# Performance work log

Hardware: AMD Instinct MI355X
Metric: run time of the kernel (lower is better)

The kernel has to match this reference:

```python
import jax, jax.numpy as jnp
import numpy as np

N_NODES = 30000
DEGREE = 16
HIDDEN = 128
MSG = 128


def setup_inputs() -> dict:
    key = jax.random.key(0)
    ks = jax.random.split(key, 16)
    coords = jax.random.normal(ks[0], (N_NODES, 3), dtype=jnp.float32)
    hidden = jax.random.normal(ks[1], (N_NODES, HIDDEN), dtype=jnp.float32)
    # fixed in-degree ring graph: unique (src,dst) pairs, in-degree == DEGREE for all nodes
    dst = jnp.repeat(jnp.arange(N_NODES, dtype=jnp.int64), DEGREE)
    off = jnp.tile(jnp.arange(1, DEGREE + 1, dtype=jnp.int64), N_NODES)
    src = (dst + off) % N_NODES
    edges = jnp.stack([src, dst], axis=0)  # [2, E]
    s = 0.05
    W1 = jax.random.normal(ks[2], (2 * HIDDEN + 1, MSG), dtype=jnp.float32) * s
    b1 = jnp.zeros((MSG,), jnp.float32)
    W2 = jax.random.normal(ks[3], (MSG, MSG), dtype=jnp.float32) * s
    b2 = jnp.zeros((MSG,), jnp.float32)
    Wa = jax.random.normal(ks[4], (MSG, 1), dtype=jnp.float32) * s
    ba = jnp.zeros((1,), jnp.float32)
    Wc1 = jax.random.normal(ks[5], (MSG, MSG), dtype=jnp.float32) * s
    bc1 = jnp.zeros((MSG,), jnp.float32)
    Wc2 = jax.random.normal(ks[6], (MSG, 1), dtype=jnp.float32) * s  # original zero-inits; random for nontrivial baseline
    Wh1 = jax.random.normal(ks[7], (HIDDEN + MSG, MSG), dtype=jnp.float32) * s
    bh1 = jnp.zeros((MSG,), jnp.float32)
    Wh2 = jax.random.normal(ks[8], (MSG, HIDDEN), dtype=jnp.float32) * s
    bh2 = jnp.zeros((HIDDEN,), jnp.float32)
    return dict(coords=coords, hidden=hidden, edges=edges, W1=W1, b1=b1, W2=W2, b2=b2,
                Wa=Wa, ba=ba, Wc1=Wc1, bc1=bc1, Wc2=Wc2, Wh1=Wh1, bh1=bh1, Wh2=Wh2, bh2=bh2)


def reference(coords, hidden, edges, W1, b1, W2, b2, Wa, ba, Wc1, bc1, Wc2, Wh1, bh1, Wh2, bh2):
    n = coords.shape[0]
    src, dst = edges[0], edges[1]
    coords_dif = coords[src] - coords[dst]                      # [E,3]
    l2 = jnp.linalg.norm(coords_dif, axis=1, keepdims=True)     # [E,1]
    x = jnp.concatenate([hidden[src], hidden[dst], l2], axis=1)  # [E, 2h+1]
    m = jnp.tanh(x @ W1 + b1)
    m = jnp.tanh(m @ W2 + b2)                                   # m_ij [E,MSG]
    m = jax.nn.sigmoid(m @ Wa + ba) * m                          # attention gate
    c = jnp.tanh(m @ Wc1 + bc1)
    c = jnp.tanh(c @ Wc2)                                       # [E,1] (Tanh since has_attention)
    coord_trans = coords_dif * c                                 # [E,3]
    # dense [N,N,*] scatter + sum over dim 0 == segment-sum over edges[1] (unique edges)
    trans_sum = jax.ops.segment_sum(coord_trans, dst, num_segments=n)  # [N,3]
    indeg = jax.ops.segment_sum(jnp.ones_like(dst, dtype=coords.dtype), dst, num_segments=n)
    coords_out = coords + trans_sum / indeg[:, None]
    m_i = jax.ops.segment_sum(m, dst, num_segments=n)            # [N,MSG]
    h = jnp.tanh(jnp.concatenate([hidden, m_i], axis=1) @ Wh1 + bh1)
    h = h @ Wh2 + bh2
    hidden_out = hidden + h
    return coords_out, hidden_out
```

## Files before the change

### kernel.cpp

```cpp
#include <hip/hip_runtime.h>
#include <hip/hip_bf16.h>
#include <math.h>


typedef __attribute__((ext_vector_type(8))) short short8;
typedef __attribute__((ext_vector_type(4))) float f32x4;
typedef __attribute__((ext_vector_type(4))) unsigned int u32x4;

#define MFMA __builtin_amdgcn_mfma_f32_16x16x32_bf16

#define OFF_W1A_HI 0
#define OFF_W1A_LO 16384
#define OFF_W1B_HI 32768
#define OFF_W1B_LO 49152
#define OFF_W2_HI  65536
#define OFF_WC1_HI 81920
#define OFF_WH1_HI 98304
#define OFF_WH1_LO 131072
#define OFF_WH2_HI 163840
#define FRAG_TOTAL 180224

__device__ __align__(16) unsigned short g_frags[FRAG_TOTAL];

#define DEVFN static __device__ __forceinline__

DEVFN unsigned short f2bf(float x) {
  unsigned int u = __float_as_uint(x);
  u += 0x7fffu + ((u >> 16) & 1u);
  return (unsigned short)(u >> 16);
}
DEVFN float bf2f(unsigned short h) { return __uint_as_float(((unsigned int)h) << 16); }

DEVFN unsigned int pk2(float a, float b) {
  __hip_bfloat162 p = __float22bfloat162_rn(make_float2(a, b));
  union { __hip_bfloat162 h; unsigned int u; } cv;
  cv.h = p;
  return cv.u;
}

DEVFN float ftanh(float x) {
  float e = exp2f(x * 2.8853900817779268f);
  return 1.0f - 2.0f * __builtin_amdgcn_rcpf(e + 1.0f);
}
DEVFN float fsigmoid(float x) {
  float e = exp2f(-x * 1.4426950408889634f);
  return __builtin_amdgcn_rcpf(1.0f + e);
}

DEVFN short8 bfrag(int off_u16, int kt, int nt, int lane) {
  return *(const short8*)(g_frags + off_u16 + (((kt << 3) + nt) << 9) + (lane << 3));
}

DEVFN short8 xs_read(const unsigned short* Xs, int row, int sbyte) {
  return *(const short8*)((const char*)Xs + row * 256 + (sbyte ^ ((row & 7) << 4)));
}
DEVFN void xs_write8(unsigned short* Xs, int row, int cl, const float* v) {
  u32x4 w;
  w[0] = pk2(v[0], v[1]); w[1] = pk2(v[2], v[3]);
  w[2] = pk2(v[4], v[5]); w[3] = pk2(v[6], v[7]);
  *(u32x4*)((char*)Xs + row * 256 + ((cl << 4) ^ ((row & 7) << 4))) = w;
}

#define ZERO_ACC1                                                      \
  _Pragma("unroll") for (int nt = 0; nt < 8; ++nt) acc[nt] = vzero;

__global__ __launch_bounds__(256) void hconv_kernel(const float* __restrict__ h,
                                                    unsigned short* __restrict__ Hh,
                                                    unsigned short* __restrict__ Hl,
                                                    int n4) {
  int i = blockIdx.x * 256 + threadIdx.x;
  if (i >= n4) return;
  f32x4 v = ((const f32x4*)h)[i];
  unsigned short hh[4], ll[4];
#pragma unroll
  for (int j = 0; j < 4; ++j) {
    hh[j] = f2bf(v[j]);
    ll[j] = f2bf(v[j] - bf2f(hh[j]));
  }
  ((uint2*)Hh)[i] = make_uint2(hh[0] | ((unsigned)hh[1] << 16), hh[2] | ((unsigned)hh[3] << 16));
  ((uint2*)Hl)[i] = make_uint2(ll[0] | ((unsigned)ll[1] << 16), ll[2] | ((unsigned)ll[3] << 16));
}

__global__ __launch_bounds__(256) void wconv_kernel(const float* __restrict__ W1,
                                                    const float* __restrict__ W2,
                                                    const float* __restrict__ Wc1,
                                                    const float* __restrict__ Wh1,
                                                    const float* __restrict__ Wh2) {
  int t = blockIdx.x * 256 + threadIdx.x;
  if (t >= 28 * 4096) return;
  int seg = t >> 12, r = t & 4095;
  int j = r & 7, lane = (r >> 3) & 63, nt = (r >> 9) & 7;
  int kg = lane >> 4, cl = lane & 15;
  const float* src; int kt, offH, offL, perm;
  if (seg < 4)       { src = W1;             kt = seg;      offH = OFF_W1A_HI; offL = OFF_W1A_LO; perm = 0; }
  else if (seg < 8)  { src = W1 + 128 * 128; kt = seg - 4;  offH = OFF_W1B_HI; offL = OFF_W1B_LO; perm = 0; }
  else if (seg < 12) { src = W2;             kt = seg - 8;  offH = OFF_W2_HI;  offL = -1;         perm = 1; }
  else if (seg < 16) { src = Wc1;            kt = seg - 12; offH = OFF_WC1_HI; offL = -1;         perm = 1; }
  else if (seg < 24) { src = Wh1;            kt = seg - 16; offH = OFF_WH1_HI; offL = OFF_WH1_LO; perm = 0; }
  else               { src = Wh2;            kt = seg - 24; offH = OFF_WH2_HI; offL = -1;         perm = 1; }
  int ke = kt * 32 + kg * 8 + j;
  int k = perm ? ((ke & 7) * 16 + (ke >> 3)) : ke;
  float w = src[k * 128 + nt * 16 + cl];
  unsigned short h = f2bf(w);
  int fi = kt * 4096 + nt * 512 + lane * 8 + j;
  g_frags[offH + fi] = h;
  if (offL >= 0) g_frags[offL + fi] = f2bf(w - bf2f(h));
}

__global__ __launch_bounds__(256) void tdst_kernel(const unsigned short* __restrict__ Hh,
                                                   const unsigned short* __restrict__ Hl,
                                                   const float* __restrict__ b1,
                                                   float* __restrict__ T, int N) {
  const int tid = threadIdx.x, wid = tid >> 6, lane = tid & 63;
  const int cl = lane & 15, kg = lane >> 4;
  const int n0 = blockIdx.x * 64 + wid * 16;
  const int row = min(n0 + cl, N - 1) << 7;
  const f32x4 vzero = {0.f, 0.f, 0.f, 0.f};
  f32x4 acc[8];
  ZERO_ACC1;
#pragma unroll
  for (int ks = 0; ks < 4; ++ks) {
    short8 ah = *(const short8*)(Hh + row + ks * 32 + kg * 8);
    short8 al = *(const short8*)(Hl + row + ks * 32 + kg * 8);
#pragma unroll
    for (int nt = 0; nt < 8; ++nt) {
      short8 bh = bfrag(OFF_W1B_HI, ks, nt, lane);
      short8 bl = bfrag(OFF_W1B_LO, ks, nt, lane);
      acc[nt] = MFMA(ah, bh, acc[nt], 0, 0, 0);
      acc[nt] = MFMA(al, bh, acc[nt], 0, 0, 0);
      acc[nt] = MFMA(ah, bl, acc[nt], 0, 0, 0);
    }
  }
#pragma unroll
  for (int nt = 0; nt < 8; ++nt) {
    float bv = b1[nt * 16 + cl];
#pragma unroll
    for (int reg = 0; reg < 4; ++reg) {
      int rw = n0 + kg * 4 + reg;
      if (rw < N) T[(size_t)rw * 128 + nt * 16 + cl] = acc[nt][reg] + bv;
    }
  }
}

__global__ __launch_bounds__(256) void edge_kernel(
    const float* __restrict__ coords, const int* __restrict__ edges,
    const float* __restrict__ W1, const float* __restrict__ b2,
    const float* __restrict__ Wa, const float* __restrict__ ba,
    const float* __restrict__ bc1, const float* __restrict__ Wc2,
    const float* __restrict__ T, const unsigned short* __restrict__ Hh,
    const unsigned short* __restrict__ Hl, unsigned short* __restrict__ Mh,
    unsigned short* __restrict__ Ml, float* __restrict__ coords_out, int E) {
  __shared__ __align__(16) unsigned short Xs[64 * 128];
  __shared__ float sb2f[128], sbc1f[128];
  __shared__ unsigned short swl2h[128], swah[128], swc2h[128];

  const int tid = threadIdx.x, wid = tid >> 6, lane = tid & 63;
  const int cl = lane & 15, kg = lane >> 4;
  const int xrow0 = wid * 16;
  const int e0 = blockIdx.x * 64 + wid * 16;

  if (tid < 128) {
    swl2h[tid] = f2bf(W1[256 * 128 + tid]);
    swah[tid] = f2bf(Wa[tid]);
    swc2h[tid] = f2bf(Wc2[tid]);
    sb2f[tid] = b2[tid];
    sbc1f[tid] = bc1[tid];
  }
  __syncthreads();

  const int dst = edges[E + e0];
  const int src = edges[e0 + cl];
  const int srcRow = src << 7;
  const float cx = coords[3 * dst], cy = coords[3 * dst + 1], cz = coords[3 * dst + 2];
  const float dx = coords[3 * src] - cx, dy = coords[3 * src + 1] - cy, dz = coords[3 * src + 2] - cz;
  const float l2 = sqrtf(dx * dx + dy * dy + dz * dz);
  const float ba_s = ba[0];

  const f32x4 vzero = {0.f, 0.f, 0.f, 0.f};
  f32x4 acc[8];
  ZERO_ACC1;

#pragma unroll
  for (int ks = 0; ks < 4; ++ks) {
    short8 ah = *(const short8*)(Hh + srcRow + ks * 32 + kg * 8);
    short8 al = *(const short8*)(Hl + srcRow + ks * 32 + kg * 8);
#pragma unroll
    for (int nt = 0; nt < 8; ++nt) {
      short8 bh = bfrag(OFF_W1A_HI, ks, nt, lane);
      short8 bl = bfrag(OFF_W1A_LO, ks, nt, lane);
      acc[nt] = MFMA(ah, bh, acc[nt], 0, 0, 0);
      acc[nt] = MFMA(al, bh, acc[nt], 0, 0, 0);
      acc[nt] = MFMA(ah, bl, acc[nt], 0, 0, 0);
    }
  }

  {
    const float* Trow = T + (size_t)dst * 128;
    float l2r[4];
#pragma unroll
    for (int reg = 0; reg < 4; ++reg) l2r[reg] = __shfl(l2, kg * 4 + reg);
    float vv[4][8];
#pragma unroll
    for (int nt = 0; nt < 8; ++nt) {
      float tv = Trow[nt * 16 + cl];
      float wl = bf2f(swl2h[nt * 16 + cl]);
#pragma unroll
      for (int reg = 0; reg < 4; ++reg)
        vv[reg][nt] = ftanh(acc[nt][reg] + tv + l2r[reg] * wl);
    }
#pragma unroll
    for (int reg = 0; reg < 4; ++reg) xs_write8(Xs, xrow0 + kg * 4 + reg, cl, vv[reg]);
  }

  ZERO_ACC1;
#pragma unroll
  for (int ks = 0; ks < 4; ++ks) {
    short8 a = xs_read(Xs, xrow0 + cl, ks * 64 + kg * 16);
#pragma unroll
    for (int nt = 0; nt < 8; ++nt) {
      short8 b = bfrag(OFF_W2_HI, ks, nt, lane);
      acc[nt] = MFMA(a, b, acc[nt], 0, 0, 0);
    }
  }

  {
    float wac[8], b2c[8];
#pragma unroll
    for (int nt = 0; nt < 8; ++nt) {
      wac[nt] = bf2f(swah[nt * 16 + cl]);
      b2c[nt] = sb2f[nt * 16 + cl];
    }
#pragma unroll
    for (int nt = 0; nt < 8; ++nt)
#pragma unroll
      for (int reg = 0; reg < 4; ++reg)
        acc[nt][reg] = ftanh(acc[nt][reg] + b2c[nt]);
    float p[4];
#pragma unroll
    for (int reg = 0; reg < 4; ++reg) {
      float s = 0.f;
#pragma unroll
      for (int nt = 0; nt < 8; ++nt) s = fmaf(acc[nt][reg], wac[nt], s);
      p[reg] = s;
    }
#pragma unroll
    for (int m = 1; m <= 8; m <<= 1)
#pragma unroll
      for (int reg = 0; reg < 4; ++reg) p[reg] += __shfl_xor(p[reg], m);
    float g[4];
#pragma unroll
    for (int reg = 0; reg < 4; ++reg) g[reg] = fsigmoid(p[reg] + ba_s);
#pragma unroll
    for (int nt = 0; nt < 8; ++nt)
#pragma unroll
      for (int reg = 0; reg < 4; ++reg) acc[nt][reg] *= g[reg];
    float cs[8];
#pragma unroll
    for (int nt = 0; nt < 8; ++nt) {
      cs[nt] = (acc[nt][0] + acc[nt][1]) + (acc[nt][2] + acc[nt][3]);
      cs[nt] += __shfl_xor(cs[nt], 16);
      cs[nt] += __shfl_xor(cs[nt], 32);
    }
    if (lane < 16) {
      size_t base = (size_t)dst * 128 + lane;
#pragma unroll
      for (int nt = 0; nt < 8; ++nt) {
        float s = cs[nt];
        unsigned short hh = f2bf(s);
        Mh[base + nt * 16] = hh;
        Ml[base + nt * 16] = f2bf(s - bf2f(hh));
      }
    }
    float vv[4][8];
#pragma unroll
    for (int nt = 0; nt < 8; ++nt)
#pragma unroll
      for (int reg = 0; reg < 4; ++reg) vv[reg][nt] = acc[nt][reg];
#pragma unroll
    for (int reg = 0; reg < 4; ++reg) xs_write8(Xs, xrow0 + kg * 4 + reg, cl, vv[reg]);
  }

  ZERO_ACC1;
#pragma unroll
  for (int ks = 0; ks < 4; ++ks) {
    short8 a = xs_read(Xs, xrow0 + cl, ks * 64 + kg * 16);
#pragma unroll
    for (int nt = 0; nt < 8; ++nt) {
      short8 b = bfrag(OFF_WC1_HI, ks, nt, lane);
      acc[nt] = MFMA(a, b, acc[nt], 0, 0, 0);
    }
  }

  {
    float wcc[8], bcc[8];
#pragma unroll
    for (int nt = 0; nt < 8; ++nt) {
      wcc[nt] = bf2f(swc2h[nt * 16 + cl]);
      bcc[nt] = sbc1f[nt * 16 + cl];
    }
    float p[4];
#pragma unroll
    for (int reg = 0; reg < 4; ++reg) {
      float s = 0.f;
#pragma unroll
      for (int nt = 0; nt < 8; ++nt)
        s = fmaf(ftanh(acc[nt][reg] + bcc[nt]), wcc[nt], s);
      p[reg] = s;
    }
#pragma unroll
    for (int m = 1; m <= 8; m <<= 1)
#pragma unroll
      for (int reg = 0; reg < 4; ++reg) p[reg] += __shfl_xor(p[reg], m);
    float st = 0.f;
#pragma unroll
    for (int reg = 0; reg < 4; ++reg) {
      int sl = kg * 4 + reg;
      float vx = __shfl(dx, sl), vy = __shfl(dy, sl), vz = __shfl(dz, sl);
      float cmp = ((cl & 3) == 1) ? vy : (((cl & 3) == 2) ? vz : vx);
      st = fmaf(cmp, ftanh(p[reg]), st);
    }
    st += __shfl_xor(st, 16);
    st += __shfl_xor(st, 32);
    if (lane < 3)
      coords_out[dst * 3 + lane] = coords[dst * 3 + lane] + st * 0.0625f;
  }
}

__global__ __launch_bounds__(256) void node_kernel(
    const float* __restrict__ hidden, const unsigned short* __restrict__ Hh,
    const unsigned short* __restrict__ Hl, const unsigned short* __restrict__ Mh,
    const unsigned short* __restrict__ Ml, const float* __restrict__ bh1,
    const float* __restrict__ bh2, float* __restrict__ hidden_out, int N) {
  __shared__ __align__(16) unsigned short Xs[64 * 128];
  const int tid = threadIdx.x, wid = tid >> 6, lane = tid & 63;
  const int cl = lane & 15, kg = lane >> 4;
  const int xrow0 = wid * 16;
  const int n0 = blockIdx.x * 64 + wid * 16;
  const int row = min(n0 + cl, N - 1) << 7;
  const f32x4 vzero = {0.f, 0.f, 0.f, 0.f};
  f32x4 acc[8];
  ZERO_ACC1;
#pragma unroll
  for (int half = 0; half < 2; ++half) {
    const unsigned short* Ph = half ? Mh : Hh;
    const unsigned short* Pl = half ? Ml : Hl;
#pragma unroll
    for (int ks = 0; ks < 4; ++ks) {
      short8 ah = *(const short8*)(Ph + row + ks * 32 + kg * 8);
      short8 al = *(const short8*)(Pl + row + ks * 32 + kg * 8);
#pragma unroll
      for (int nt = 0; nt < 8; ++nt) {
        short8 bh = bfrag(OFF_WH1_HI, half * 4 + ks, nt, lane);
        short8 bl = bfrag(OFF_WH1_LO, half * 4 + ks, nt, lane);
        acc[nt] = MFMA(ah, bh, acc[nt], 0, 0, 0);
        acc[nt] = MFMA(al, bh, acc[nt], 0, 0, 0);
        acc[nt] = MFMA(ah, bl, acc[nt], 0, 0, 0);
      }
    }
  }
  {
    float vv[4][8];
#pragma unroll
    for (int nt = 0; nt < 8; ++nt) {
      float bv = bh1[nt * 16 + cl];
#pragma unroll
      for (int reg = 0; reg < 4; ++reg) vv[reg][nt] = ftanh(acc[nt][reg] + bv);
    }
#pragma unroll
    for (int reg = 0; reg < 4; ++reg) xs_write8(Xs, xrow0 + kg * 4 + reg, cl, vv[reg]);
  }
  ZERO_ACC1;
#pragma unroll
  for (int ks = 0; ks < 4; ++ks) {
    short8 a = xs_read(Xs, xrow0 + cl, ks * 64 + kg * 16);
#pragma unroll
    for (int nt = 0; nt < 8; ++nt) {
      short8 b = bfrag(OFF_WH2_HI, ks, nt, lane);
      acc[nt] = MFMA(a, b, acc[nt], 0, 0, 0);
    }
  }
#pragma unroll
  for (int nt = 0; nt < 8; ++nt) {
    float bv = bh2[nt * 16 + cl];
#pragma unroll
    for (int reg = 0; reg < 4; ++reg) {
      int rw = n0 + kg * 4 + reg;
      if (rw < N) {
        size_t o = (size_t)rw * 128 + nt * 16 + cl;
        hidden_out[o] = hidden[o] + acc[nt][reg] + bv;
      }
    }
  }
}

extern "C" void kernel_launch(void* const* d_in, const int* in_sizes, int n_in,
                              void* d_out, int out_size, void* d_ws, size_t ws_size,
                              hipStream_t stream) {
  const float* coords = (const float*)d_in[0];
  const float* hidden = (const float*)d_in[1];
  const int* edges = (const int*)d_in[2];
  const float* W1 = (const float*)d_in[3];
  const float* b1 = (const float*)d_in[4];
  const float* W2 = (const float*)d_in[5];
  const float* b2 = (const float*)d_in[6];
  const float* Wa = (const float*)d_in[7];
  const float* ba = (const float*)d_in[8];
  const float* Wc1 = (const float*)d_in[9];
  const float* bc1 = (const float*)d_in[10];
  const float* Wc2 = (const float*)d_in[11];
  const float* Wh1 = (const float*)d_in[12];
  const float* bh1 = (const float*)d_in[13];
  const float* Wh2 = (const float*)d_in[14];
  const float* bh2 = (const float*)d_in[15];

  const int N = in_sizes[0] / 3;
  const int E = in_sizes[2] / 2;

  float* T = (float*)d_ws;
  unsigned short* Hh = (unsigned short*)(T + (size_t)N * 128);
  unsigned short* Hl = Hh + (size_t)N * 128;
  unsigned short* Mh = Hl + (size_t)N * 128;
  unsigned short* Ml = Mh + (size_t)N * 128;
  float* coords_out = (float*)d_out;
  float* hidden_out = coords_out + (size_t)N * 3;

  const int n4 = N * 32;
  hconv_kernel<<<(n4 + 255) / 256, 256, 0, stream>>>(hidden, Hh, Hl, n4);
  wconv_kernel<<<448, 256, 0, stream>>>(W1, W2, Wc1, Wh1, Wh2);
  const int nb = (N + 63) / 64;
  tdst_kernel<<<nb, 256, 0, stream>>>(Hh, Hl, b1, T, N);
  edge_kernel<<<E / 64, 256, 0, stream>>>(coords, edges, W1, b2, Wa, ba, bc1, Wc2,
                                          T, Hh, Hl, Mh, Ml, coords_out, E);
  node_kernel<<<nb, 256, 0, stream>>>(hidden, Hh, Hl, Mh, Ml, bh1, bh2, hidden_out, N);
}
```

Measured before the change: 307.3 us.

## Precompute per-node source projection and fold hidden bf16 split into GEMM kernels

The hidden[src] @ W1a product is now computed once per node in a combined S/T kernel instead of once per edge, so the edge kernel only gathers precomputed S rows and skips the first 3-pass split-bf16 GEMM. The separate hidden-to-bf16 conversion kernel is removed and the hi/lo split is done inline from fp32 loads. The node kernel is reorganized to use 32 rows per block with waves splitting output columns, which needs an added block barrier. Small scalar weights are kept in fp32 and tanh/sigmoid use raw exp/rcp asm. The cost is an extra N x 128 fp32 buffer that is written and then gathered per edge.

```diff
diff --git a/kernel.cpp b/kernel.cpp
--- a/kernel.cpp
+++ b/kernel.cpp
@@ -38,13 +38,37 @@
   return cv.u;
 }
 
+DEVFN float fexp2(float x) {
+  float r;
+  asm volatile("v_exp_f32 %0, %1" : "=v"(r) : "v"(x));
+  return r;
+}
+DEVFN float frcp(float x) {
+  float r;
+  asm volatile("v_rcp_f32 %0, %1" : "=v"(r) : "v"(x));
+  return r;
+}
 DEVFN float ftanh(float x) {
-  float e = exp2f(x * 2.8853900817779268f);
-  return 1.0f - 2.0f * __builtin_amdgcn_rcpf(e + 1.0f);
+  return 1.0f - 2.0f * frcp(fexp2(x * 2.8853900817779268f) + 1.0f);
 }
 DEVFN float fsigmoid(float x) {
-  float e = exp2f(-x * 1.4426950408889634f);
-  return __builtin_amdgcn_rcpf(1.0f + e);
+  return frcp(1.0f + fexp2(-x * 1.4426950408889634f));
+}
+
+DEVFN void mk8(const float* __restrict__ x, short8& hi, short8& lo) {
+  unsigned int hp[4], lp[4];
+#pragma unroll
+  for (int q = 0; q < 4; ++q) hp[q] = pk2(x[2 * q], x[2 * q + 1]);
+#pragma unroll
+  for (int q = 0; q < 4; ++q) {
+    float f0 = __uint_as_float(hp[q] << 16);
+    float f1 = __uint_as_float(hp[q] & 0xffff0000u);
+    lp[q] = pk2(x[2 * q] - f0, x[2 * q + 1] - f1);
+  }
+  union { u32x4 u; short8 s; } ch, clo;
+  ch.u[0] = hp[0]; ch.u[1] = hp[1]; ch.u[2] = hp[2]; ch.u[3] = hp[3];
+  clo.u[0] = lp[0]; clo.u[1] = lp[1]; clo.u[2] = lp[2]; clo.u[3] = lp[3];
+  hi = ch.s; lo = clo.s;
 }
 
 DEVFN short8 bfrag(int off_u16, int kt, int nt, int lane) {
@@ -60,26 +84,14 @@
   w[2] = pk2(v[4], v[5]); w[3] = pk2(v[6], v[7]);
   *(u32x4*)((char*)Xs + row * 256 + ((cl << 4) ^ ((row & 7) << 4))) = w;
 }
-
-#define ZERO_ACC1                                                      \
-  _Pragma("unroll") for (int nt = 0; nt < 8; ++nt) acc[nt] = vzero;
-
-__global__ __launch_bounds__(256) void hconv_kernel(const float* __restrict__ h,
-                                                    unsigned short* __restrict__ Hh,
-                                                    unsigned short* __restrict__ Hl,
-                                                    int n4) {
-  int i = blockIdx.x * 256 + threadIdx.x;
-  if (i >= n4) return;
-  f32x4 v = ((const f32x4*)h)[i];
-  unsigned short hh[4], ll[4];
-#pragma unroll
-  for (int j = 0; j < 4; ++j) {
-    hh[j] = f2bf(v[j]);
-    ll[j] = f2bf(v[j] - bf2f(hh[j]));
-  }
-  ((uint2*)Hh)[i] = make_uint2(hh[0] | ((unsigned)hh[1] << 16), hh[2] | ((unsigned)hh[3] << 16));
-  ((uint2*)Hl)[i] = make_uint2(ll[0] | ((unsigned)ll[1] << 16), ll[2] | ((unsigned)ll[3] << 16));
-}
+DEVFN void xs_write4(unsigned short* Xs, int row, int byte0, const float* v) {
+  uint2 w;
+  w.x = pk2(v[0], v[1]); w.y = pk2(v[2], v[3]);
+  *(uint2*)((char*)Xs + row * 256 + (byte0 ^ ((row & 7) << 4))) = w;
+}
+
+#define ZERO8 { _Pragma("unroll") for (int nt = 0; nt < 8; ++nt) acc[nt] = vzero; }
+#define ZERO4(a) { _Pragma("unroll") for (int q = 0; q < 4; ++q) (a)[q] = vzero; }
 
 __global__ __launch_bounds__(256) void wconv_kernel(const float* __restrict__ W1,
                                                     const float* __restrict__ W2,
@@ -107,37 +119,52 @@
   if (offL >= 0) g_frags[offL + fi] = f2bf(w - bf2f(h));
 }
 
-__global__ __launch_bounds__(256) void tdst_kernel(const unsigned short* __restrict__ Hh,
-                                                   const unsigned short* __restrict__ Hl,
-                                                   const float* __restrict__ b1,
-                                                   float* __restrict__ T, int N) {
+__global__ __launch_bounds__(256) void st_kernel(const float* __restrict__ hidden,
+                                                 const float* __restrict__ b1,
+                                                 float* __restrict__ S,
+                                                 float* __restrict__ T, int N) {
   const int tid = threadIdx.x, wid = tid >> 6, lane = tid & 63;
   const int cl = lane & 15, kg = lane >> 4;
-  const int n0 = blockIdx.x * 64 + wid * 16;
-  const int row = min(n0 + cl, N - 1) << 7;
+  const int rg = wid >> 1, nh = wid & 1;
+  const int n0 = blockIdx.x * 32 + rg * 16;
+  const float* Arow = hidden + ((size_t)min(n0 + cl, N - 1) << 7);
   const f32x4 vzero = {0.f, 0.f, 0.f, 0.f};
-  f32x4 acc[8];
-  ZERO_ACC1;
+  f32x4 accS[4], accT[4];
+  ZERO4(accS); ZERO4(accT);
 #pragma unroll
   for (int ks = 0; ks < 4; ++ks) {
-    short8 ah = *(const short8*)(Hh + row + ks * 32 + kg * 8);
-    short8 al = *(const short8*)(Hl + row + ks * 32 + kg * 8);
-#pragma unroll
-    for (int nt = 0; nt < 8; ++nt) {
-      short8 bh = bfrag(OFF_W1B_HI, ks, nt, lane);
-      short8 bl = bfrag(OFF_W1B_LO, ks, nt, lane);
-      acc[nt] = MFMA(ah, bh, acc[nt], 0, 0, 0);
-      acc[nt] = MFMA(al, bh, acc[nt], 0, 0, 0);
-      acc[nt] = MFMA(ah, bl, acc[nt], 0, 0, 0);
-    }
-  }
-#pragma unroll
-  for (int nt = 0; nt < 8; ++nt) {
+    float x[8];
+    *(f32x4*)&x[0] = *(const f32x4*)(Arow + ks * 32 + kg * 8);
+    *(f32x4*)&x[4] = *(const f32x4*)(Arow + ks * 32 + kg * 8 + 4);
+    short8 ah, al;
+    mk8(x, ah, al);
+#pragma unroll
+    for (int q = 0; q < 4; ++q) {
+      int nt = nh * 4 + q;
+      short8 bh = bfrag(OFF_W1A_HI, ks, nt, lane);
+      short8 bl = bfrag(OFF_W1A_LO, ks, nt, lane);
+      accS[q] = MFMA(ah, bh, accS[q], 0, 0, 0);
+      accS[q] = MFMA(al, bh, accS[q], 0, 0, 0);
+      accS[q] = MFMA(ah, bl, accS[q], 0, 0, 0);
+      bh = bfrag(OFF_W1B_HI, ks, nt, lane);
+      bl = bfrag(OFF_W1B_LO, ks, nt, lane);
+      accT[q] = MFMA(ah, bh, accT[q], 0, 0, 0);
+      accT[q] = MFMA(al, bh, accT[q], 0, 0, 0);
+      accT[q] = MFMA(ah, bl, accT[q], 0, 0, 0);
+    }
+  }
+#pragma unroll
+  for (int q = 0; q < 4; ++q) {
+    int nt = nh * 4 + q;
     float bv = b1[nt * 16 + cl];
 #pragma unroll
     for (int reg = 0; reg < 4; ++reg) {
       int rw = n0 + kg * 4 + reg;
-      if (rw < N) T[(size_t)rw * 128 + nt * 16 + cl] = acc[nt][reg] + bv;
+      if (rw < N) {
+        size_t o = (size_t)rw * 128 + nt * 16 + cl;
+        S[o] = accS[q][reg];
+        T[o] = accT[q][reg] + bv;
+      }
     }
   }
 }
@@ -147,12 +174,11 @@
     const float* __restrict__ W1, const float* __restrict__ b2,
     const float* __restrict__ Wa, const float* __restrict__ ba,
     const float* __restrict__ bc1, const float* __restrict__ Wc2,
-    const float* __restrict__ T, const unsigned short* __restrict__ Hh,
-    const unsigned short* __restrict__ Hl, unsigned short* __restrict__ Mh,
-    unsigned short* __restrict__ Ml, float* __restrict__ coords_out, int E) {
+    const float* __restrict__ T, const float* __restrict__ S,
+    unsigned short* __restrict__ Mh, unsigned short* __restrict__ Ml,
+    float* __restrict__ coords_out, int E) {
   __shared__ __align__(16) unsigned short Xs[64 * 128];
-  __shared__ float sb2f[128], sbc1f[128];
-  __shared__ unsigned short swl2h[128], swah[128], swc2h[128];
+  __shared__ float swl2f[128], swaf[128], swc2f[128], sb2f[128], sbc1f[128];
 
   const int tid = threadIdx.x, wid = tid >> 6, lane = tid & 63;
   const int cl = lane & 15, kg = lane >> 4;
@@ -160,9 +186,9 @@
   const int e0 = blockIdx.x * 64 + wid * 16;
 
   if (tid < 128) {
-    swl2h[tid] = f2bf(W1[256 * 128 + tid]);
-    swah[tid] = f2bf(Wa[tid]);
-    swc2h[tid] = f2bf(Wc2[tid]);
+    swl2f[tid] = W1[256 * 128 + tid];
+    swaf[tid] = Wa[tid];
+    swc2f[tid] = Wc2[tid];
     sb2f[tid] = b2[tid];
     sbc1f[tid] = bc1[tid];
   }
@@ -170,7 +196,6 @@
 
   const int dst = edges[E + e0];
   const int src = edges[e0 + cl];
-  const int srcRow = src << 7;
   const float cx = coords[3 * dst], cy = coords[3 * dst + 1], cz = coords[3 * dst + 2];
   const float dx = coords[3 * src] - cx, dy = coords[3 * src + 1] - cy, dz = coords[3 * src + 2] - cz;
   const float l2 = sqrtf(dx * dx + dy * dy + dz * dz);
@@ -178,41 +203,31 @@
 
   const f32x4 vzero = {0.f, 0.f, 0.f, 0.f};
   f32x4 acc[8];
-  ZERO_ACC1;
-
-#pragma unroll
-  for (int ks = 0; ks < 4; ++ks) {
-    short8 ah = *(const short8*)(Hh + srcRow + ks * 32 + kg * 8);
-    short8 al = *(const short8*)(Hl + srcRow + ks * 32 + kg * 8);
-#pragma unroll
-    for (int nt = 0; nt < 8; ++nt) {
-      short8 bh = bfrag(OFF_W1A_HI, ks, nt, lane);
-      short8 bl = bfrag(OFF_W1A_LO, ks, nt, lane);
-      acc[nt] = MFMA(ah, bh, acc[nt], 0, 0, 0);
-      acc[nt] = MFMA(al, bh, acc[nt], 0, 0, 0);
-      acc[nt] = MFMA(ah, bl, acc[nt], 0, 0, 0);
-    }
-  }
 
   {
     const float* Trow = T + (size_t)dst * 128;
+    const float* Srow[4];
     float l2r[4];
 #pragma unroll
-    for (int reg = 0; reg < 4; ++reg) l2r[reg] = __shfl(l2, kg * 4 + reg);
+    for (int reg = 0; reg < 4; ++reg) {
+      Srow[reg] = S + ((size_t)__shfl(src, kg * 4 + reg) << 7);
+      l2r[reg] = __shfl(l2, kg * 4 + reg);
+    }
     float vv[4][8];
 #pragma unroll
     for (int nt = 0; nt < 8; ++nt) {
-      float tv = Trow[nt * 16 + cl];
-      float wl = bf2f(swl2h[nt * 16 + cl]);
+      const int c = nt * 16 + cl;
+      float tv = Trow[c];
+      float wl = swl2f[c];
 #pragma unroll
       for (int reg = 0; reg < 4; ++reg)
-        vv[reg][nt] = ftanh(acc[nt][reg] + tv + l2r[reg] * wl);
+        vv[reg][nt] = ftanh(Srow[reg][c] + tv + l2r[reg] * wl);
     }
 #pragma unroll
     for (int reg = 0; reg < 4; ++reg) xs_write8(Xs, xrow0 + kg * 4 + reg, cl, vv[reg]);
   }
 
-  ZERO_ACC1;
+  ZERO8;
 #pragma unroll
   for (int ks = 0; ks < 4; ++ks) {
     short8 a = xs_read(Xs, xrow0 + cl, ks * 64 + kg * 16);
@@ -227,7 +242,7 @@
     float wac[8], b2c[8];
 #pragma unroll
     for (int nt = 0; nt < 8; ++nt) {
-      wac[nt] = bf2f(swah[nt * 16 + cl]);
+      wac[nt] = swaf[nt * 16 + cl];
       b2c[nt] = sb2f[nt * 16 + cl];
     }
 #pragma unroll
@@ -280,7 +295,7 @@
     for (int reg = 0; reg < 4; ++reg) xs_write8(Xs, xrow0 + kg * 4 + reg, cl, vv[reg]);
   }
 
-  ZERO_ACC1;
+  ZERO8;
 #pragma unroll
   for (int ks = 0; ks < 4; ++ks) {
     short8 a = xs_read(Xs, xrow0 + cl, ks * 64 + kg * 16);
@@ -295,7 +310,7 @@
     float wcc[8], bcc[8];
 #pragma unroll
     for (int nt = 0; nt < 8; ++nt) {
-      wcc[nt] = bf2f(swc2h[nt * 16 + cl]);
+      wcc[nt] = swc2f[nt * 16 + cl];
       bcc[nt] = sbc1f[nt * 16 + cl];
     }
     float p[4];
@@ -327,67 +342,88 @@
 }
 
 __global__ __launch_bounds__(256) void node_kernel(
-    const float* __restrict__ hidden, const unsigned short* __restrict__ Hh,
-    const unsigned short* __restrict__ Hl, const unsigned short* __restrict__ Mh,
+    const float* __restrict__ hidden, const unsigned short* __restrict__ Mh,
     const unsigned short* __restrict__ Ml, const float* __restrict__ bh1,
     const float* __restrict__ bh2, float* __restrict__ hidden_out, int N) {
-  __shared__ __align__(16) unsigned short Xs[64 * 128];
+  __shared__ __align__(16) unsigned short Xs[32 * 128];
   const int tid = threadIdx.x, wid = tid >> 6, lane = tid & 63;
   const int cl = lane & 15, kg = lane >> 4;
-  const int xrow0 = wid * 16;
-  const int n0 = blockIdx.x * 64 + wid * 16;
-  const int row = min(n0 + cl, N - 1) << 7;
+  const int rg = wid >> 1, nh = wid & 1;
+  const int n0 = blockIdx.x * 32 + rg * 16;
+  const int rmin = min(n0 + cl, N - 1);
   const f32x4 vzero = {0.f, 0.f, 0.f, 0.f};
-  f32x4 acc[8];
-  ZERO_ACC1;
-#pragma unroll
-  for (int half = 0; half < 2; ++half) {
-    const unsigned short* Ph = half ? Mh : Hh;
-    const unsigned short* Pl = half ? Ml : Hl;
+  f32x4 acc[4];
+  ZERO4(acc);
+  {
+    const float* Arow = hidden + ((size_t)rmin << 7);
 #pragma unroll
     for (int ks = 0; ks < 4; ++ks) {
-      short8 ah = *(const short8*)(Ph + row + ks * 32 + kg * 8);
-      short8 al = *(const short8*)(Pl + row + ks * 32 + kg * 8);
-#pragma unroll
-      for (int nt = 0; nt < 8; ++nt) {
-        short8 bh = bfrag(OFF_WH1_HI, half * 4 + ks, nt, lane);
-        short8 bl = bfrag(OFF_WH1_LO, half * 4 + ks, nt, lane);
-        acc[nt] = MFMA(ah, bh, acc[nt], 0, 0, 0);
-        acc[nt] = MFMA(al, bh, acc[nt], 0, 0, 0);
-        acc[nt] = MFMA(ah, bl, acc[nt], 0, 0, 0);
+      float x[8];
+      *(f32x4*)&x[0] = *(const f32x4*)(Arow + ks * 32 + kg * 8);
+      *(f32x4*)&x[4] = *(const f32x4*)(Arow + ks * 32 + kg * 8 + 4);
+      short8 ah, al;
+      mk8(x, ah, al);
+#pragma unroll
+      for (int q = 0; q < 4; ++q) {
+        int nt = nh * 4 + q;
+        short8 bh = bfrag(OFF_WH1_HI, ks, nt, lane);
+        short8 bl = bfrag(OFF_WH1_LO, ks, nt, lane);
+        acc[q] = MFMA(ah, bh, acc[q], 0, 0, 0);
+        acc[q] = MFMA(al, bh, acc[q], 0, 0, 0);
+        acc[q] = MFMA(ah, bl, acc[q], 0, 0, 0);
       }
     }
   }
   {
-    float vv[4][8];
-#pragma unroll
-    for (int nt = 0; nt < 8; ++nt) {
-      float bv = bh1[nt * 16 + cl];
-#pragma unroll
-      for (int reg = 0; reg < 4; ++reg) vv[reg][nt] = ftanh(acc[nt][reg] + bv);
-    }
-#pragma unroll
-    for (int reg = 0; reg < 4; ++reg) xs_write8(Xs, xrow0 + kg * 4 + reg, cl, vv[reg]);
-  }
-  ZERO_ACC1;
+    const int prow = rmin << 7;
+#pragma unroll
+    for (int ks = 0; ks < 4; ++ks) {
+      short8 ah = *(const short8*)(Mh + prow + ks * 32 + kg * 8);
+      short8 al = *(const short8*)(Ml + prow + ks * 32 + kg * 8);
+#pragma unroll
+      for (int q = 0; q < 4; ++q) {
+        int nt = nh * 4 + q;
+        short8 bh = bfrag(OFF_WH1_HI, 4 + ks, nt, lane);
+        short8 bl = bfrag(OFF_WH1_LO, 4 + ks, nt, lane);
+        acc[q] = MFMA(ah, bh, acc[q], 0, 0, 0);
+        acc[q] = MFMA(al, bh, acc[q], 0, 0, 0);
+        acc[q] = MFMA(ah, bl, acc[q], 0, 0, 0);
+      }
+    }
+  }
+  {
+    float vv[4][4];
+#pragma unroll
+    for (int q = 0; q < 4; ++q) {
+      float bv = bh1[(nh * 4 + q) * 16 + cl];
+#pragma unroll
+      for (int reg = 0; reg < 4; ++reg) vv[reg][q] = ftanh(acc[q][reg] + bv);
+    }
+#pragma unroll
+    for (int reg = 0; reg < 4; ++reg)
+      xs_write4(Xs, rg * 16 + kg * 4 + reg, cl * 16 + nh * 8, vv[reg]);
+  }
+  __syncthreads();
+  ZERO4(acc);
 #pragma unroll
   for (int ks = 0; ks < 4; ++ks) {
-    short8 a = xs_read(Xs, xrow0 + cl, ks * 64 + kg * 16);
-#pragma unroll
-    for (int nt = 0; nt < 8; ++nt) {
-      short8 b = bfrag(OFF_WH2_HI, ks, nt, lane);
-      acc[nt] = MFMA(a, b, acc[nt], 0, 0, 0);
-    }
-  }
-#pragma unroll
-  for (int nt = 0; nt < 8; ++nt) {
+    short8 a = xs_read(Xs, rg * 16 + cl, ks * 64 + kg * 16);
+#pragma unroll
+    for (int q = 0; q < 4; ++q) {
+      short8 b = bfrag(OFF_WH2_HI, ks, nh * 4 + q, lane);
+      acc[q] = MFMA(a, b, acc[q], 0, 0, 0);
+    }
+  }
+#pragma unroll
+  for (int q = 0; q < 4; ++q) {
+    int nt = nh * 4 + q;
     float bv = bh2[nt * 16 + cl];
 #pragma unroll
     for (int reg = 0; reg < 4; ++reg) {
       int rw = n0 + kg * 4 + reg;
       if (rw < N) {
         size_t o = (size_t)rw * 128 + nt * 16 + cl;
-        hidden_out[o] = hidden[o] + acc[nt][reg] + bv;
+        hidden_out[o] = hidden[o] + acc[q][reg] + bv;
       }
     }
   }
@@ -417,19 +453,16 @@
   const int E = in_sizes[2] / 2;
 
   float* T = (float*)d_ws;
-  unsigned short* Hh = (unsigned short*)(T + (size_t)N * 128);
-  unsigned short* Hl = Hh + (size_t)N * 128;
-  unsigned short* Mh = Hl + (size_t)N * 128;
+  float* S = T + (size_t)N * 128;
+  unsigned short* Mh = (unsigned short*)(S + (size_t)N * 128);
   unsigned short* Ml = Mh + (size_t)N * 128;
   float* coords_out = (float*)d_out;
   float* hidden_out = coords_out + (size_t)N * 3;
 
-  const int n4 = N * 32;
-  hconv_kernel<<<(n4 + 255) / 256, 256, 0, stream>>>(hidden, Hh, Hl, n4);
   wconv_kernel<<<448, 256, 0, stream>>>(W1, W2, Wc1, Wh1, Wh2);
-  const int nb = (N + 63) / 64;
-  tdst_kernel<<<nb, 256, 0, stream>>>(Hh, Hl, b1, T, N);
+  const int nb32 = (N + 31) / 32;
+  st_kernel<<<nb32, 256, 0, stream>>>(hidden, b1, S, T, N);
   edge_kernel<<<E / 64, 256, 0, stream>>>(coords, edges, W1, b2, Wa, ba, bc1, Wc2,
-                                          T, Hh, Hl, Mh, Ml, coords_out, E);
-  node_kernel<<<nb, 256, 0, stream>>>(hidden, Hh, Hl, Mh, Ml, bh1, bh2, hidden_out, N);
-}
+                                          T, S, Mh, Ml, coords_out, E);
+  node_kernel<<<nb32, 256, 0, stream>>>(hidden, Mh, Ml, bh1, bh2, hidden_out, N);
+}
```

Result: faster. 286.9 us (-6.7%).
